# Optimization experiments

Measured on AMD Instinct MI355X. Metric: run time of the kernel, lower is better.

## Reference

```python
import jax, jax.numpy as jnp
import numpy as np

NEG_BIG = -9e15
ALPHA = 0.2  # LeakyReLU negative slope


def setup_inputs() -> dict:
    key = jax.random.key(0)
    k1, k2, k3, k4 = jax.random.split(key, 4)
    N, F_in, F_out = 10000, 512, 64
    inp = {
        "input": jax.random.normal(k1, (N, F_in), dtype=jnp.float32),
        "W": jax.random.normal(k2, (F_in, F_out), dtype=jnp.float32) * (1.414 / np.sqrt(F_in)),
        "a": jax.random.normal(k3, (2 * F_out, 1), dtype=jnp.float32) * 0.1,
        "adj": jax.random.randint(k4, (N, N), 0, 2, dtype=jnp.int32),
    }
    return inp


def reference(input, W, a, adj):
    # h: [N, F'] projected features
    h = input @ W
    F_out = h.shape[1]
    # e_ij = LeakyReLU([h_i || h_j] . a) == LeakyReLU(h@a1 + (h@a2)^T)
    # (mathematically identical, avoids materializing [N, N, 2F'])
    a1, a2 = a[:F_out], a[F_out:]          # each [F', 1]
    e = (h @ a1) + (h @ a2).T              # [N, N]
    e = jax.nn.leaky_relu(e, negative_slope=ALPHA)
    # adjacency-masked softmax over neighbors j
    e = jnp.where(adj > 0, e, NEG_BIG)
    attention = jax.nn.softmax(e, axis=1)  # [N, N]
    # weighted aggregation
    h_prime = attention @ h                # [N, F']
    # concat=True -> ELU activation
    return jax.nn.elu(h_prime)
```

## Files before the change

kernel.cpp:

```cpp
#include <hip/hip_runtime.h>
#include <hip/hip_bf16.h>

#define N_NODES 10000
#define FIN 512
#define FOUT 64
#define NP 10016
#define LEAKY_ALPHA 0.2f
#define TOTAL_STEPS 313

typedef __attribute__((ext_vector_type(8))) short short8;
typedef __attribute__((ext_vector_type(4))) float f32x4;
typedef __attribute__((ext_vector_type(8))) __bf16 bf16x8;

static __device__ __forceinline__ unsigned short f2bf(float f) {
  unsigned u = __builtin_bit_cast(unsigned, f);
  u += 0x7FFFu + ((u >> 16) & 1u);
  return (unsigned short)(u >> 16);
}
static __device__ __forceinline__ float bf2f(unsigned short s) {
  unsigned u = ((unsigned)s) << 16;
  return __builtin_bit_cast(float, u);
}
static __device__ __forceinline__ unsigned enc_f32(float f) {
  unsigned u = __builtin_bit_cast(unsigned, f);
  return (u & 0x80000000u) ? ~u : (u | 0x80000000u);
}
static __device__ __forceinline__ float dec_f32(unsigned u) {
  unsigned b = (u & 0x80000000u) ? (u & 0x7FFFFFFFu) : ~u;
  return __builtin_bit_cast(float, b);
}

__global__ __launch_bounds__(64) void gat_h(
    const float* __restrict__ input, const float* __restrict__ W,
    const float* __restrict__ a, float* __restrict__ s1,
    float* __restrict__ s2, unsigned short* __restrict__ hbT,
    unsigned int* __restrict__ maxbits) {
  __shared__ float in_lds[8 * FIN];
  const int l = threadIdx.x;
  const int rb = blockIdx.x * 8;

  const float4* src = (const float4*)(input + (size_t)rb * FIN);
  float4* dst = (float4*)in_lds;
#pragma unroll
  for (int v = 0; v < 16; ++v) dst[l + 64 * v] = src[l + 64 * v];
  __syncthreads();

  float acc[8] = {0.f, 0.f, 0.f, 0.f, 0.f, 0.f, 0.f, 0.f};
  for (int k4 = 0; k4 < FIN / 4; ++k4) {
    float w0 = W[(k4 * 4 + 0) * FOUT + l];
    float w1 = W[(k4 * 4 + 1) * FOUT + l];
    float w2 = W[(k4 * 4 + 2) * FOUT + l];
    float w3 = W[(k4 * 4 + 3) * FOUT + l];
#pragma unroll
    for (int r = 0; r < 8; ++r) {
      float4 iv = *(const float4*)&in_lds[r * FIN + k4 * 4];
      acc[r] = fmaf(iv.x, w0, fmaf(iv.y, w1, fmaf(iv.z, w2, fmaf(iv.w, w3, acc[r]))));
    }
  }

  short8 pk;
#pragma unroll
  for (int r = 0; r < 8; ++r) pk[r] = (short)f2bf(acc[r]);
  *(short8*)(hbT + (size_t)l * NP + rb) = pk;

  const float a1l = a[l], a2l = a[FOUT + l];
  float m1 = -1e30f, m2 = -1e30f;
#pragma unroll
  for (int r = 0; r < 8; ++r) {
    float v1 = acc[r] * a1l, v2 = acc[r] * a2l;
#pragma unroll
    for (int off = 32; off > 0; off >>= 1) {
      v1 += __shfl_xor(v1, off);
      v2 += __shfl_xor(v2, off);
    }
    if (l == 0) { s1[rb + r] = v1; s2[rb + r] = v2; }
    m1 = fmaxf(m1, v1);
    m2 = fmaxf(m2, v2);
  }
  if (l == 0) {
    atomicMax(maxbits + 0, enc_f32(m1));
    atomicMax(maxbits + 1, enc_f32(m2));
  }
}

__global__ __launch_bounds__(64) void gat_attn(
    const int* __restrict__ adj, const float* __restrict__ s1,
    const float* __restrict__ s2, const unsigned short* __restrict__ hbT,
    const unsigned int* __restrict__ maxbits,
    float* __restrict__ num_part, float* __restrict__ den_part,
    int steps_per_chunk) {
  const int l = threadIdx.x;
  const int r = l & 15;
  const int g = l >> 4;
  const int kb = g * 8;
  const int row_base = blockIdx.x * 16;
  const int split = blockIdx.y;

  const float msum = dec_f32(maxbits[0]) + dec_f32(maxbits[1]);
  const float m = (msum > 0.f) ? msum : LEAKY_ALPHA * msum;

  int sb = split * steps_per_chunk;
  int se = sb + steps_per_chunk;
  if (se > TOTAL_STEPS) se = TOTAL_STEPS;
  bool has_tail = false;
  if (se == TOTAL_STEPS) { has_tail = true; se = TOTAL_STEPS - 1; }

  const float s1r = s1[row_base + r];
  const int* __restrict__ adjp = adj + (size_t)(row_base + r) * N_NODES;
  const unsigned short* __restrict__ bp = hbT + (size_t)r * NP;

  f32x4 acc0 = {0.f, 0.f, 0.f, 0.f};
  f32x4 acc1 = {0.f, 0.f, 0.f, 0.f};
  f32x4 acc2 = {0.f, 0.f, 0.f, 0.f};
  f32x4 acc3 = {0.f, 0.f, 0.f, 0.f};
  float den_acc = 0.f;

  for (int t = sb; t < se; ++t) {
    const int j = t * 32 + kb;
    int4 av0 = *(const int4*)(adjp + j);
    int4 av1 = *(const int4*)(adjp + j + 4);
    float4 sv0 = *(const float4*)(s2 + j);
    float4 sv1 = *(const float4*)(s2 + j + 4);
    short8 b0 = *(const short8*)(bp + j);
    short8 b1 = *(const short8*)(bp + 16 * NP + j);
    short8 b2 = *(const short8*)(bp + 32 * NP + j);
    short8 b3 = *(const short8*)(bp + 48 * NP + j);

    float sef[8] = {sv0.x, sv0.y, sv0.z, sv0.w, sv1.x, sv1.y, sv1.z, sv1.w};
    int ad[8] = {av0.x, av0.y, av0.z, av0.w, av1.x, av1.y, av1.z, av1.w};
    short8 af;
#pragma unroll
    for (int e = 0; e < 8; ++e) {
      float ee = s1r + sef[e];
      ee = (ee >= 0.f) ? ee : LEAKY_ALPHA * ee;
      float w = (ad[e] > 0) ? __expf(ee - m) : 0.f;
      unsigned short wb = f2bf(w);
      af[e] = (short)wb;
      den_acc += bf2f(wb);
    }
    bf16x8 av = __builtin_bit_cast(bf16x8, af);
    acc0 = __builtin_amdgcn_mfma_f32_16x16x32_bf16(av, __builtin_bit_cast(bf16x8, b0), acc0, 0, 0, 0);
    acc1 = __builtin_amdgcn_mfma_f32_16x16x32_bf16(av, __builtin_bit_cast(bf16x8, b1), acc1, 0, 0, 0);
    acc2 = __builtin_amdgcn_mfma_f32_16x16x32_bf16(av, __builtin_bit_cast(bf16x8, b2), acc2, 0, 0, 0);
    acc3 = __builtin_amdgcn_mfma_f32_16x16x32_bf16(av, __builtin_bit_cast(bf16x8, b3), acc3, 0, 0, 0);
  }

  if (has_tail) {
    short8 af = {0, 0, 0, 0, 0, 0, 0, 0};
    short8 b0 = {0, 0, 0, 0, 0, 0, 0, 0};
    short8 b1 = {0, 0, 0, 0, 0, 0, 0, 0};
    short8 b2 = {0, 0, 0, 0, 0, 0, 0, 0};
    short8 b3 = {0, 0, 0, 0, 0, 0, 0, 0};
    if (g < 2) {
      const int j = 9984 + kb;
      int4 av0 = *(const int4*)(adjp + j);
      int4 av1 = *(const int4*)(adjp + j + 4);
      float4 sv0 = *(const float4*)(s2 + j);
      float4 sv1 = *(const float4*)(s2 + j + 4);
      b0 = *(const short8*)(bp + j);
      b1 = *(const short8*)(bp + 16 * NP + j);
      b2 = *(const short8*)(bp + 32 * NP + j);
      b3 = *(const short8*)(bp + 48 * NP + j);
      float sef[8] = {sv0.x, sv0.y, sv0.z, sv0.w, sv1.x, sv1.y, sv1.z, sv1.w};
      int ad[8] = {av0.x, av0.y, av0.z, av0.w, av1.x, av1.y, av1.z, av1.w};
#pragma unroll
      for (int e = 0; e < 8; ++e) {
        float ee = s1r + sef[e];
        ee = (ee >= 0.f) ? ee : LEAKY_ALPHA * ee;
        float w = (ad[e] > 0) ? __expf(ee - m) : 0.f;
        unsigned short wb = f2bf(w);
        af[e] = (short)wb;
        den_acc += bf2f(wb);
      }
    }
    bf16x8 av = __builtin_bit_cast(bf16x8, af);
    acc0 = __builtin_amdgcn_mfma_f32_16x16x32_bf16(av, __builtin_bit_cast(bf16x8, b0), acc0, 0, 0, 0);
    acc1 = __builtin_amdgcn_mfma_f32_16x16x32_bf16(av, __builtin_bit_cast(bf16x8, b1), acc1, 0, 0, 0);
    acc2 = __builtin_amdgcn_mfma_f32_16x16x32_bf16(av, __builtin_bit_cast(bf16x8, b2), acc2, 0, 0, 0);
    acc3 = __builtin_amdgcn_mfma_f32_16x16x32_bf16(av, __builtin_bit_cast(bf16x8, b3), acc3, 0, 0, 0);
  }

  den_acc += __shfl_xor(den_acc, 16);
  den_acc += __shfl_xor(den_acc, 32);
  if (l < 16) den_part[(size_t)split * N_NODES + row_base + r] = den_acc;

  float* np_ = num_part + ((size_t)split * N_NODES + row_base) * FOUT;
#pragma unroll
  for (int q = 0; q < 4; ++q) {
    const int orow = g * 4 + q;
    np_[orow * FOUT + 0 + r] = acc0[q];
    np_[orow * FOUT + 16 + r] = acc1[q];
    np_[orow * FOUT + 32 + r] = acc2[q];
    np_[orow * FOUT + 48 + r] = acc3[q];
  }
}

__global__ __launch_bounds__(256) void gat_out(
    const float* __restrict__ num_part, const float* __restrict__ den_part,
    const unsigned short* __restrict__ hbT, float* __restrict__ out, int S) {
  const int idx = blockIdx.x * 256 + threadIdx.x;
  if (idx >= N_NODES * FOUT) return;
  const int i = idx >> 6, f = idx & 63;
  float den = 0.f, num = 0.f;
  for (int s = 0; s < S; ++s) {
    den += den_part[(size_t)s * N_NODES + i];
    num += num_part[(size_t)s * N_NODES * FOUT + idx];
  }
  float v;
  if (den > 0.f) {
    v = num / den;
  } else {
    float sum = 0.f;
    for (int j = 0; j < N_NODES; ++j) sum += bf2f(hbT[(size_t)f * NP + j]);
    v = sum / (float)N_NODES;
  }
  out[idx] = (v > 0.f) ? v : (__expf(v) - 1.f);
}

extern "C" void kernel_launch(void* const* d_in, const int* in_sizes, int n_in,
                              void* d_out, int out_size, void* d_ws, size_t ws_size,
                              hipStream_t stream) {
  const float* input = (const float*)d_in[0];
  const float* W = (const float*)d_in[1];
  const float* a = (const float*)d_in[2];
  const int* adj = (const int*)d_in[3];
  float* out = (float*)d_out;

  int S = 4;
  {
    size_t need4 = (size_t)4 * N_NODES * FOUT * 4 + (size_t)4 * N_NODES * 4 + 64 +
                   (size_t)N_NODES * 4 + (size_t)NP * 4 + (size_t)FOUT * NP * 2 + 256;
    if (ws_size < need4) S = 1;
  }

  char* p = (char*)d_ws;
  float* num_part = (float*)p;               p += (size_t)S * N_NODES * FOUT * 4;
  float* den_part = (float*)p;               p += (size_t)S * N_NODES * 4;
  unsigned int* maxbits = (unsigned int*)p;  p += 64;
  float* s1 = (float*)p;                     p += (size_t)N_NODES * 4;
  float* s2 = (float*)p;                     p += (size_t)NP * 4;
  unsigned short* hbT = (unsigned short*)p;

  size_t zero_bytes = (size_t)S * N_NODES * FOUT * 4 + (size_t)S * N_NODES * 4 + 8;
  hipMemsetAsync(d_ws, 0, zero_bytes, stream);

  hipLaunchKernelGGL(gat_h, dim3(N_NODES / 8), dim3(64), 0, stream,
                     input, W, a, s1, s2, hbT, maxbits);

  int steps_per_chunk = (TOTAL_STEPS + S - 1) / S;
  hipLaunchKernelGGL(gat_attn, dim3(N_NODES / 16, S), dim3(64), 0, stream,
                     adj, s1, s2, hbT, maxbits, num_part, den_part, steps_per_chunk);

  hipLaunchKernelGGL(gat_out, dim3((N_NODES * FOUT + 255) / 256), dim3(256), 0, stream,
                     num_part, den_part, hbT, out, S);
}
```

Measured before the change: 684.7 us.

## Pack waves into 256-thread blocks, use more splits, MFMA denominator, vectorize reduction

The attention kernel now packs four 16-row tiles per 256-thread block and splits the neighbour dimension eight ways instead of four, to put more waves in flight on a kernel bound by streaming adj. The softmax denominator is computed by an extra MFMA against a ones vector instead of per-lane adds and shuffles. Weights are packed in pairs with fmaxf-based LeakyReLU. The large workspace memset is cut to the 8-byte max slot, since partials are fully overwritten, and the output kernel reads and writes float4. More splits mean more partial traffic in the reduction kernel.

```diff
diff --git a/kernel.cpp b/kernel.cpp
--- a/kernel.cpp
+++ b/kernel.cpp
@@ -5,12 +5,14 @@
 #define FIN 512
 #define FOUT 64
 #define NP 10016
-#define LEAKY_ALPHA 0.2f
 #define TOTAL_STEPS 313
+#define N_TILES 625
+#define SPLITS 8
 
 typedef __attribute__((ext_vector_type(8))) short short8;
 typedef __attribute__((ext_vector_type(4))) float f32x4;
 typedef __attribute__((ext_vector_type(8))) __bf16 bf16x8;
+typedef __attribute__((ext_vector_type(4))) unsigned int uint4v;
 
 static __device__ __forceinline__ unsigned short f2bf(float f) {
   unsigned u = __builtin_bit_cast(unsigned, f);
@@ -28,6 +30,16 @@
 static __device__ __forceinline__ float dec_f32(unsigned u) {
   unsigned b = (u & 0x80000000u) ? (u & 0x7FFFFFFFu) : ~u;
   return __builtin_bit_cast(float, b);
+}
+
+static __device__ __forceinline__ unsigned wpair(float s1r, float sA, float sB,
+                                                 int adA, int adB, float m) {
+  float eA = s1r + sA, eB = s1r + sB;
+  eA = fmaxf(eA, 0.2f * eA);
+  eB = fmaxf(eB, 0.2f * eB);
+  float wA = (adA > 0) ? __expf(eA - m) : 0.f;
+  float wB = (adB > 0) ? __expf(eB - m) : 0.f;
+  return ((unsigned)f2bf(wB) << 16) | (unsigned)f2bf(wA);
 }
 
 __global__ __launch_bounds__(64) void gat_h(
@@ -83,21 +95,26 @@
   }
 }
 
-__global__ __launch_bounds__(64) void gat_attn(
+__global__ __launch_bounds__(256, 8) void gat_attn(
     const int* __restrict__ adj, const float* __restrict__ s1,
     const float* __restrict__ s2, const unsigned short* __restrict__ hbT,
     const unsigned int* __restrict__ maxbits,
     float* __restrict__ num_part, float* __restrict__ den_part,
     int steps_per_chunk) {
-  const int l = threadIdx.x;
+  const int tid = threadIdx.x;
+  const int wave = tid >> 6;
+  const int l = tid & 63;
+  const int tile = blockIdx.x * 4 + wave;
+  if (tile >= N_TILES) return;
+
   const int r = l & 15;
   const int g = l >> 4;
   const int kb = g * 8;
-  const int row_base = blockIdx.x * 16;
+  const int row_base = tile * 16;
   const int split = blockIdx.y;
 
   const float msum = dec_f32(maxbits[0]) + dec_f32(maxbits[1]);
-  const float m = (msum > 0.f) ? msum : LEAKY_ALPHA * msum;
+  const float m = fmaxf(msum, 0.2f * msum);
 
   int sb = split * steps_per_chunk;
   int se = sb + steps_per_chunk;
@@ -109,80 +126,72 @@
   const int* __restrict__ adjp = adj + (size_t)(row_base + r) * N_NODES;
   const unsigned short* __restrict__ bp = hbT + (size_t)r * NP;
 
+  short8 ones_s;
+#pragma unroll
+  for (int e = 0; e < 8; ++e) ones_s[e] = (short)0x3F80;
+  const bf16x8 onesv = __builtin_bit_cast(bf16x8, ones_s);
+
   f32x4 acc0 = {0.f, 0.f, 0.f, 0.f};
   f32x4 acc1 = {0.f, 0.f, 0.f, 0.f};
   f32x4 acc2 = {0.f, 0.f, 0.f, 0.f};
   f32x4 acc3 = {0.f, 0.f, 0.f, 0.f};
-  float den_acc = 0.f;
+  f32x4 accd = {0.f, 0.f, 0.f, 0.f};
 
   for (int t = sb; t < se; ++t) {
     const int j = t * 32 + kb;
-    int4 av0 = *(const int4*)(adjp + j);
-    int4 av1 = *(const int4*)(adjp + j + 4);
-    float4 sv0 = *(const float4*)(s2 + j);
-    float4 sv1 = *(const float4*)(s2 + j + 4);
+    int4 a0 = *(const int4*)(adjp + j);
+    int4 a1 = *(const int4*)(adjp + j + 4);
+    float4 s0 = *(const float4*)(s2 + j);
+    float4 sv = *(const float4*)(s2 + j + 4);
+    uint4v au;
+    au.x = wpair(s1r, s0.x, s0.y, a0.x, a0.y, m);
+    au.y = wpair(s1r, s0.z, s0.w, a0.z, a0.w, m);
+    au.z = wpair(s1r, sv.x, sv.y, a1.x, a1.y, m);
+    au.w = wpair(s1r, sv.z, sv.w, a1.z, a1.w, m);
+    bf16x8 av = __builtin_bit_cast(bf16x8, au);
     short8 b0 = *(const short8*)(bp + j);
     short8 b1 = *(const short8*)(bp + 16 * NP + j);
     short8 b2 = *(const short8*)(bp + 32 * NP + j);
     short8 b3 = *(const short8*)(bp + 48 * NP + j);
-
-    float sef[8] = {sv0.x, sv0.y, sv0.z, sv0.w, sv1.x, sv1.y, sv1.z, sv1.w};
-    int ad[8] = {av0.x, av0.y, av0.z, av0.w, av1.x, av1.y, av1.z, av1.w};
-    short8 af;
-#pragma unroll
-    for (int e = 0; e < 8; ++e) {
-      float ee = s1r + sef[e];
-      ee = (ee >= 0.f) ? ee : LEAKY_ALPHA * ee;
-      float w = (ad[e] > 0) ? __expf(ee - m) : 0.f;
-      unsigned short wb = f2bf(w);
-      af[e] = (short)wb;
-      den_acc += bf2f(wb);
-    }
-    bf16x8 av = __builtin_bit_cast(bf16x8, af);
     acc0 = __builtin_amdgcn_mfma_f32_16x16x32_bf16(av, __builtin_bit_cast(bf16x8, b0), acc0, 0, 0, 0);
     acc1 = __builtin_amdgcn_mfma_f32_16x16x32_bf16(av, __builtin_bit_cast(bf16x8, b1), acc1, 0, 0, 0);
     acc2 = __builtin_amdgcn_mfma_f32_16x16x32_bf16(av, __builtin_bit_cast(bf16x8, b2), acc2, 0, 0, 0);
     acc3 = __builtin_amdgcn_mfma_f32_16x16x32_bf16(av, __builtin_bit_cast(bf16x8, b3), acc3, 0, 0, 0);
+    accd = __builtin_amdgcn_mfma_f32_16x16x32_bf16(av, onesv, accd, 0, 0, 0);
   }
 
   if (has_tail) {
-    short8 af = {0, 0, 0, 0, 0, 0, 0, 0};
-    short8 b0 = {0, 0, 0, 0, 0, 0, 0, 0};
-    short8 b1 = {0, 0, 0, 0, 0, 0, 0, 0};
-    short8 b2 = {0, 0, 0, 0, 0, 0, 0, 0};
-    short8 b3 = {0, 0, 0, 0, 0, 0, 0, 0};
+    uint4v au = {0u, 0u, 0u, 0u};
+    short8 b0 = {0,0,0,0,0,0,0,0}, b1 = {0,0,0,0,0,0,0,0};
+    short8 b2 = {0,0,0,0,0,0,0,0}, b3 = {0,0,0,0,0,0,0,0};
     if (g < 2) {
       const int j = 9984 + kb;
-      int4 av0 = *(const int4*)(adjp + j);
-      int4 av1 = *(const int4*)(adjp + j + 4);
-      float4 sv0 = *(const float4*)(s2 + j);
-      float4 sv1 = *(const float4*)(s2 + j + 4);
+      int4 a0 = *(const int4*)(adjp + j);
+      int4 a1 = *(const int4*)(adjp + j + 4);
+      float4 s0 = *(const float4*)(s2 + j);
+      float4 sv = *(const float4*)(s2 + j + 4);
       b0 = *(const short8*)(bp + j);
       b1 = *(const short8*)(bp + 16 * NP + j);
       b2 = *(const short8*)(bp + 32 * NP + j);
       b3 = *(const short8*)(bp + 48 * NP + j);
-      float sef[8] = {sv0.x, sv0.y, sv0.z, sv0.w, sv1.x, sv1.y, sv1.z, sv1.w};
-      int ad[8] = {av0.x, av0.y, av0.z, av0.w, av1.x, av1.y, av1.z, av1.w};
-#pragma unroll
-      for (int e = 0; e < 8; ++e) {
-        float ee = s1r + sef[e];
-        ee = (ee >= 0.f) ? ee : LEAKY_ALPHA * ee;
-        float w = (ad[e] > 0) ? __expf(ee - m) : 0.f;
-        unsigned short wb = f2bf(w);
-        af[e] = (short)wb;
-        den_acc += bf2f(wb);
-      }
-    }
-    bf16x8 av = __builtin_bit_cast(bf16x8, af);
+      au.x = wpair(s1r, s0.x, s0.y, a0.x, a0.y, m);
+      au.y = wpair(s1r, s0.z, s0.w, a0.z, a0.w, m);
+      au.z = wpair(s1r, sv.x, sv.y, a1.x, a1.y, m);
+      au.w = wpair(s1r, sv.z, sv.w, a1.z, a1.w, m);
+    }
+    bf16x8 av = __builtin_bit_cast(bf16x8, au);
     acc0 = __builtin_amdgcn_mfma_f32_16x16x32_bf16(av, __builtin_bit_cast(bf16x8, b0), acc0, 0, 0, 0);
     acc1 = __builtin_amdgcn_mfma_f32_16x16x32_bf16(av, __builtin_bit_cast(bf16x8, b1), acc1, 0, 0, 0);
     acc2 = __builtin_amdgcn_mfma_f32_16x16x32_bf16(av, __builtin_bit_cast(bf16x8, b2), acc2, 0, 0, 0);
     acc3 = __builtin_amdgcn_mfma_f32_16x16x32_bf16(av, __builtin_bit_cast(bf16x8, b3), acc3, 0, 0, 0);
-  }
-
-  den_acc += __shfl_xor(den_acc, 16);
-  den_acc += __shfl_xor(den_acc, 32);
-  if (l < 16) den_part[(size_t)split * N_NODES + row_base + r] = den_acc;
+    accd = __builtin_amdgcn_mfma_f32_16x16x32_bf16(av, onesv, accd, 0, 0, 0);
+  }
+
+  if (r == 0) {
+#pragma unroll
+    for (int q = 0; q < 4; ++q)
+      den_part[(size_t)split * N_NODES + row_base + g * 4 + q] = accd[q];
+  }
 
   float* np_ = num_part + ((size_t)split * N_NODES + row_base) * FOUT;
 #pragma unroll
@@ -198,23 +207,36 @@
 __global__ __launch_bounds__(256) void gat_out(
     const float* __restrict__ num_part, const float* __restrict__ den_part,
     const unsigned short* __restrict__ hbT, float* __restrict__ out, int S) {
-  const int idx = blockIdx.x * 256 + threadIdx.x;
-  if (idx >= N_NODES * FOUT) return;
-  const int i = idx >> 6, f = idx & 63;
-  float den = 0.f, num = 0.f;
+  const int q = blockIdx.x * 256 + threadIdx.x;
+  if (q >= N_NODES * FOUT / 4) return;
+  const int i = q >> 4;
+  const int f4 = (q & 15) * 4;
+  float den = 0.f;
+  float4 num = {0.f, 0.f, 0.f, 0.f};
   for (int s = 0; s < S; ++s) {
     den += den_part[(size_t)s * N_NODES + i];
-    num += num_part[(size_t)s * N_NODES * FOUT + idx];
-  }
-  float v;
+    float4 v = *(const float4*)(num_part + ((size_t)s * N_NODES + i) * FOUT + f4);
+    num.x += v.x; num.y += v.y; num.z += v.z; num.w += v.w;
+  }
+  float4 res;
   if (den > 0.f) {
-    v = num / den;
+    res.x = num.x / den; res.y = num.y / den; res.z = num.z / den; res.w = num.w / den;
   } else {
-    float sum = 0.f;
-    for (int j = 0; j < N_NODES; ++j) sum += bf2f(hbT[(size_t)f * NP + j]);
-    v = sum / (float)N_NODES;
-  }
-  out[idx] = (v > 0.f) ? v : (__expf(v) - 1.f);
+    float s0 = 0.f, s1 = 0.f, s2 = 0.f, s3 = 0.f;
+    for (int j = 0; j < N_NODES; ++j) {
+      s0 += bf2f(hbT[(size_t)(f4 + 0) * NP + j]);
+      s1 += bf2f(hbT[(size_t)(f4 + 1) * NP + j]);
+      s2 += bf2f(hbT[(size_t)(f4 + 2) * NP + j]);
+      s3 += bf2f(hbT[(size_t)(f4 + 3) * NP + j]);
+    }
+    res.x = s0 / (float)N_NODES; res.y = s1 / (float)N_NODES;
+    res.z = s2 / (float)N_NODES; res.w = s3 / (float)N_NODES;
+  }
+  res.x = (res.x > 0.f) ? res.x : (__expf(res.x) - 1.f);
+  res.y = (res.y > 0.f) ? res.y : (__expf(res.y) - 1.f);
+  res.z = (res.z > 0.f) ? res.z : (__expf(res.z) - 1.f);
+  res.w = (res.w > 0.f) ? res.w : (__expf(res.w) - 1.f);
+  *(float4*)(out + (size_t)q * 4) = res;
 }
 
 extern "C" void kernel_launch(void* const* d_in, const int* in_sizes, int n_in,
@@ -226,31 +248,27 @@
   const int* adj = (const int*)d_in[3];
   float* out = (float*)d_out;
 
-  int S = 4;
-  {
-    size_t need4 = (size_t)4 * N_NODES * FOUT * 4 + (size_t)4 * N_NODES * 4 + 64 +
-                   (size_t)N_NODES * 4 + (size_t)NP * 4 + (size_t)FOUT * NP * 2 + 256;
-    if (ws_size < need4) S = 1;
-  }
+  const size_t fixed = 64 + (size_t)N_NODES * 4 + (size_t)NP * 4 + (size_t)FOUT * NP * 2 + 256;
+  int S = SPLITS;
+  if (ws_size < fixed + (size_t)SPLITS * N_NODES * (FOUT * 4 + 4)) S = 1;
 
   char* p = (char*)d_ws;
-  float* num_part = (float*)p;               p += (size_t)S * N_NODES * FOUT * 4;
-  float* den_part = (float*)p;               p += (size_t)S * N_NODES * 4;
   unsigned int* maxbits = (unsigned int*)p;  p += 64;
   float* s1 = (float*)p;                     p += (size_t)N_NODES * 4;
   float* s2 = (float*)p;                     p += (size_t)NP * 4;
-  unsigned short* hbT = (unsigned short*)p;
-
-  size_t zero_bytes = (size_t)S * N_NODES * FOUT * 4 + (size_t)S * N_NODES * 4 + 8;
-  hipMemsetAsync(d_ws, 0, zero_bytes, stream);
+  unsigned short* hbT = (unsigned short*)p;  p += (size_t)FOUT * NP * 2;
+  float* num_part = (float*)p;               p += (size_t)S * N_NODES * FOUT * 4;
+  float* den_part = (float*)p;
+
+  (void)hipMemsetAsync(maxbits, 0, 8, stream);
 
   hipLaunchKernelGGL(gat_h, dim3(N_NODES / 8), dim3(64), 0, stream,
                      input, W, a, s1, s2, hbT, maxbits);
 
   int steps_per_chunk = (TOTAL_STEPS + S - 1) / S;
-  hipLaunchKernelGGL(gat_attn, dim3(N_NODES / 16, S), dim3(64), 0, stream,
+  hipLaunchKernelGGL(gat_attn, dim3((N_TILES + 3) / 4, S), dim3(256), 0, stream,
                      adj, s1, s2, hbT, maxbits, num_part, den_part, steps_per_chunk);
 
-  hipLaunchKernelGGL(gat_out, dim3((N_NODES * FOUT + 255) / 256), dim3(256), 0, stream,
+  hipLaunchKernelGGL(gat_out, dim3((N_NODES * FOUT / 4 + 255) / 256), dim3(256), 0, stream,
                      num_part, den_part, hbT, out, S);
 }
```

New measurement: 665.6 us. -2.8%, faster.
